# Performance work log

Measured on AMD Instinct MI355X. Metric: run time of the kernel, lower is better.

The kernel has to match this reference:

```python
import jax, jax.numpy as jnp
import numpy as np
import math

# ---- module hyperparameters (from init_kwargs) ----
N = 3            # polynomial points per segment
SEGMENTS = 512   # piecewise segments over [-1, 1] (length = 2.0)
ROTATIONS = 4    # -> 2*ROTATIONS stripe directions
WIDTH = 512
HEIGHT = 512
MAX_DIM = max(WIDTH, HEIGHT)
RATIO = MAX_DIM / (MAX_DIM + 1)
NUM_POS = 2 * ROTATIONS
NW = SEGMENTS * (N - 1) + 1  # continuous piecewise weights per channel

# Chebyshev-Lobatto interpolation points on [-1, 1]
CHEB = (-np.cos(np.pi * np.arange(N) / (N - 1))).astype(np.float32)


def make_positions():
    """Rotated stripe position maps, [2*ROTATIONS, WIDTH, HEIGHT], precomputed buffers."""
    xv, yv = np.meshgrid(np.arange(WIDTH), np.arange(HEIGHT), indexing='ij')
    xv = xv.astype(np.float32)
    yv = yv.astype(np.float32)
    pos = []
    for i in range(ROTATIONS):
        theta = math.pi / 2.0 * (i / ROTATIONS)
        cx, cy = math.cos(theta), math.sin(theta)
        for sgn in (1.0, -1.0):  # r1 = cx*x + cy*y, r2 = cx*x - cy*y
            r = cx * xv + sgn * cy * yv
            rmin, rmax = r.min(), r.max()
            dr = rmax - rmin
            r = ((r - rmin) * RATIO / dr - 0.5) * MAX_DIM
            pos.append(r)
    return np.stack(pos, 0).astype(np.float32)


POSITIONS = jnp.asarray(make_positions())  # [8, W, H] constant buffer


def lagrange_basis(t):
    """Lagrange basis at Chebyshev-Lobatto points; t [...], returns [..., N]."""
    bs = []
    for k in range(N):
        b = jnp.ones_like(t)
        for j in range(N):
            if j != k:
                b = b * (t - CHEB[j]) / (CHEB[k] - CHEB[j])
        bs.append(b)
    return jnp.stack(bs, axis=-1)


def piecewise_shared(xin, w):
    """Continuous piecewise Lagrange polynomial, weights shared across positions.
    xin: [B, C, L] in ~[-1, 1]; w: [C, NW]. Returns [B, C, L]."""
    xs = (xin + 1.0) * (0.5 * SEGMENTS)              # segment-space coordinate
    sid = jnp.clip(jnp.floor(xs), 0.0, SEGMENTS - 1)  # segment index (clamped)
    t = 2.0 * (xs - sid) - 1.0                        # local coord in [-1, 1]
    sid = sid.astype(jnp.int32)
    widx = sid[..., None] * (N - 1) + jnp.arange(N)   # [B, C, L, N] weight gather idx
    cidx = jnp.arange(w.shape[0])[None, :, None, None]
    wg = w[cidx, widx]                                # [B, C, L, N]
    return jnp.sum(lagrange_basis(t) * wg, axis=-1)


def setup_inputs() -> dict:
    key = jax.random.key(0)
    k1, k2 = jax.random.split(key)
    x = jax.random.normal(k1, (16, 3, WIDTH, HEIGHT), dtype=jnp.float32)
    weights = jax.random.normal(k2, (NUM_POS, 3, NW), dtype=jnp.float32)  # weight_magnitude=1
    return {"x": x, "weights": weights}


def reference(x, weights):
    B, C, W, H = x.shape
    accum = jnp.zeros((B, C, W * H), dtype=x.dtype)
    for i in range(NUM_POS):
        # position_encode: pixel value perturbs its stripe position, then rescale to [-1,1]
        dl = (0.5 * x + POSITIONS[i]) / (0.5 * MAX_DIM)  # [B, C, W, H]
        dl = dl.reshape(B, C, W * H)
        accum = accum + piecewise_shared(dl, weights[i])
    accum = accum / NUM_POS
    return accum.reshape(x.shape)
```

## Files before the change

kernel.cpp:

```cpp
#include <hip/hip_runtime.h>
#include <math.h>


#define WDIM 512
#define HDIM 512
#define SEGS 512
#define NPOS 8
#define NTAB 7
#define NW   1025
#define CCH  3

#define THREADS 512
#define TILE_X 128
#define TILE_Y 64
#define KITER  4
#define TILES_PER_SLICE ((WDIM / TILE_X) * (HDIM / TILE_Y))

struct Params {
    float ax[NPOS];
    float ay[NPOS];
    float c0[NPOS];
};

union HalfPack {
    unsigned int u;
    _Float16 h[2];
};

__global__ __launch_bounds__(THREADS, 6)
void stripe_poly_kernel(const float* __restrict__ x,
                        const float* __restrict__ w,
                        float* __restrict__ out,
                        Params P)
{
    __shared__ uint2 lut[NTAB][SEGS];

    const int slice = blockIdx.x / TILES_PER_SLICE;
    const int tile  = blockIdx.x % TILES_PER_SLICE;
    const int ch    = slice % CCH;
    const int bx    = (tile >> 3) * TILE_X;
    const int by    = (tile & 7) * TILE_Y;

    const int tid  = threadIdx.x;
    const int wv   = tid >> 6;
    const int lane = tid & 63;
    const int px0  = bx + (wv >> 2) * 16 + (lane >> 2);
    const int py   = by + (wv & 3) * 16 + (lane & 3) * 4;
    const float yf = (float)py;

    const size_t slice_off = (size_t)slice * (WDIM * HDIM);
    const size_t pbase = slice_off + (size_t)px0 * HDIM + py;

    const float4 xin0 = *(const float4*)(x + pbase);
    const float4 xin1 = *(const float4*)(x + pbase + (size_t)(1 * 32) * HDIM);
    const float4 xin2 = *(const float4*)(x + pbase + (size_t)(2 * 32) * HDIM);
    const float4 xin3 = *(const float4*)(x + pbase + (size_t)(3 * 32) * HDIM);

    for (int idx = threadIdx.x; idx < NTAB * SEGS; idx += THREADS) {
        const int m = idx >> 9;
        const int s = idx & (SEGS - 1);
        float w0, w1, w2;
        if (m == 0) {
            const float* wa = w + (size_t)(0 * CCH + ch) * NW + 2 * s;
            const float* wb = w + (size_t)(1 * CCH + ch) * NW + 2 * s;
            w0 = wa[0] + wb[0]; w1 = wa[1] + wb[1]; w2 = wa[2] + wb[2];
        } else {
            const float* wp = w + (size_t)((m + 1) * CCH + ch) * NW + 2 * s;
            w0 = wp[0]; w1 = wp[1]; w2 = wp[2];
        }
        const float a0 = 0.125f * w0;
        const float a1 = 0.125f * (fmaf(4.0f, w1, -w2) - 3.0f * w0);
        const float a2 = 0.25f  * (w0 - 2.0f * w1 + w2);
        HalfPack hp;
        hp.h[0] = (_Float16)a1;
        hp.h[1] = (_Float16)a2;
        lut[m][s] = make_uint2(__float_as_uint(a0), hp.u);
    }

    float gy[NTAB];
    #pragma unroll
    for (int i = 0; i < NTAB; ++i) {
        const int pi = (i == 0) ? 0 : (i + 1);
        gy[i] = fmaf(P.ay[pi], yf, P.c0[pi]);
    }

    __syncthreads();

    #pragma unroll
    for (int k = 0; k < KITER; ++k) {
        const size_t pk = pbase + (size_t)(k * 32) * HDIM;
        const float xf = (float)(px0 + k * 32);
        const float4 xk = (k == 0) ? xin0 : (k == 1) ? xin1 : (k == 2) ? xin2 : xin3;
        const float xv[4] = {xk.x, xk.y, xk.z, xk.w};
        float acc[4]  = {0.f, 0.f, 0.f, 0.f};
        float accC[4] = {0.f, 0.f, 0.f, 0.f};

        #pragma unroll
        for (int i = 0; i < NTAB; ++i) {
            const int pi = (i == 0) ? 0 : (i + 1);
            const float ay = P.ay[pi];
            const float g  = fmaf(P.ax[pi], xf, gy[i]);
            float gj[4];
            gj[0] = g;
            gj[1] = g + ay;
            gj[2] = gj[1] + ay;
            gj[3] = gj[2] + ay;
            #pragma unroll
            for (int j = 0; j < 4; ++j) {
                const float xs = fmaf(0.5f, xv[j], gj[j]);
                float sf = floorf(xs);
                sf = fminf(fmaxf(sf, 0.0f), (float)(SEGS - 1));
                const int s = (int)sf;
                const float d = xs - sf;
                const uint2 v = lut[i][s];
                HalfPack hp; hp.u = v.y;
                const float u = fmaf(d, (float)hp.h[1], (float)hp.h[0]);
                accC[j] += __uint_as_float(v.x);
                acc[j]   = fmaf(d, u, acc[j]);
            }
        }

        float4 o;
        o.x = acc[0] + accC[0];
        o.y = acc[1] + accC[1];
        o.z = acc[2] + accC[2];
        o.w = acc[3] + accC[3];
        *(float4*)(out + pk) = o;
    }
}

extern "C" void kernel_launch(void* const* d_in, const int* in_sizes, int n_in,
                              void* d_out, int out_size, void* d_ws, size_t ws_size,
                              hipStream_t stream)
{
    const float* x = (const float*)d_in[0];
    const float* w = (const float*)d_in[1];
    float* out = (float*)d_out;

    Params P;
    const double ratio_f = (double)(float)(512.0 / 513.0);
    for (int i = 0; i < 4; ++i) {
        const double theta = (M_PI * 0.5) * ((double)i / 4.0);
        const float a   = (float)cos(theta);
        const float cyf = (float)sin(theta);
        for (int sg = 0; sg < 2; ++sg) {
            const float b = (sg == 0) ? cyf : -cyf;
            const float ax511 = a * 511.0f;
            const float by511 = b * 511.0f;
            float rmin, rmax;
            if (sg == 0) { rmin = 0.0f;  rmax = ax511 + by511; }
            else         { rmin = by511; rmax = ax511; }
            const float dr = rmax - rmin;
            const double K = 512.0 * ratio_f / (double)dr;
            const int pi = 2 * i + sg;
            P.ax[pi] = (float)(K * (double)a);
            P.ay[pi] = (float)(K * (double)b);
            P.c0[pi] = (float)(-K * (double)rmin);
        }
    }

    const int slices = in_sizes[0] / (WDIM * HDIM);
    const int blocks = slices * TILES_PER_SLICE;
    stripe_poly_kernel<<<blocks, THREADS, 0, stream>>>(x, w, out, P);
}
```

Measured before the change: 119.6 us.

## Switch to fixed 1024-block grid that walks channel-grouped patches and restages LUT

Replaces the one-block-per-tile grid with a fixed grid of 1024 blocks. Each block processes 48 consecutive 16x16 patches ordered channel-major, so the coefficient LUT is built once per block and rebuilt only when the channel changes. Each iteration prefetches the next patch's input while computing the current one. The aim is to amortize the LUT staging from global weights over more pixels and to raise occupancy (launch bound 8). The trade-offs are that the patch count and channel layout are hardcoded for 16x3 slices, and the loop gains occasional extra barriers where a channel boundary falls inside a block.

```diff
diff --git a/kernel.cpp b/kernel.cpp
--- a/kernel.cpp
+++ b/kernel.cpp
@@ -11,10 +11,10 @@
 #define CCH  3
 
 #define THREADS 512
-#define TILE_X 128
-#define TILE_Y 64
-#define KITER  4
-#define TILES_PER_SLICE ((WDIM / TILE_X) * (HDIM / TILE_Y))
+#define BLOCKS  1024
+#define PER_BLK 48
+#define KITER   (PER_BLK / 8)
+#define PATCH_PER_CH 16384
 
 struct Params {
     float ax[NPOS];
@@ -27,7 +27,7 @@
     _Float16 h[2];
 };
 
-__global__ __launch_bounds__(THREADS, 6)
+__global__ __launch_bounds__(THREADS, 8)
 void stripe_poly_kernel(const float* __restrict__ x,
                         const float* __restrict__ w,
                         float* __restrict__ out,
@@ -35,63 +35,73 @@
 {
     __shared__ uint2 lut[NTAB][SEGS];
 
-    const int slice = blockIdx.x / TILES_PER_SLICE;
-    const int tile  = blockIdx.x % TILES_PER_SLICE;
-    const int ch    = slice % CCH;
-    const int bx    = (tile >> 3) * TILE_X;
-    const int by    = (tile & 7) * TILE_Y;
-
     const int tid  = threadIdx.x;
     const int wv   = tid >> 6;
     const int lane = tid & 63;
-    const int px0  = bx + (wv >> 2) * 16 + (lane >> 2);
-    const int py   = by + (wv & 3) * 16 + (lane & 3) * 4;
-    const float yf = (float)py;
+    const int plx  = lane >> 2;
+    const int ply  = (lane & 3) * 4;
 
-    const size_t slice_off = (size_t)slice * (WDIM * HDIM);
-    const size_t pbase = slice_off + (size_t)px0 * HDIM + py;
+    const int qbase = blockIdx.x * PER_BLK;
 
-    const float4 xin0 = *(const float4*)(x + pbase);
-    const float4 xin1 = *(const float4*)(x + pbase + (size_t)(1 * 32) * HDIM);
-    const float4 xin2 = *(const float4*)(x + pbase + (size_t)(2 * 32) * HDIM);
-    const float4 xin3 = *(const float4*)(x + pbase + (size_t)(3 * 32) * HDIM);
+    auto stage = [&](int ch) {
+        for (int idx = tid; idx < NTAB * SEGS; idx += THREADS) {
+            const int m = idx >> 9;
+            const int s = idx & (SEGS - 1);
+            float w0, w1, w2;
+            if (m == 0) {
+                const float* wa = w + (size_t)(0 * CCH + ch) * NW + 2 * s;
+                const float* wb = w + (size_t)(1 * CCH + ch) * NW + 2 * s;
+                w0 = wa[0] + wb[0]; w1 = wa[1] + wb[1]; w2 = wa[2] + wb[2];
+            } else {
+                const float* wp = w + (size_t)((m + 1) * CCH + ch) * NW + 2 * s;
+                w0 = wp[0]; w1 = wp[1]; w2 = wp[2];
+            }
+            const float a0 = 0.125f * w0;
+            const float a1 = 0.125f * (fmaf(4.0f, w1, -w2) - 3.0f * w0);
+            const float a2 = 0.25f  * (w0 - 2.0f * w1 + w2);
+            HalfPack hp;
+            hp.h[0] = (_Float16)a1;
+            hp.h[1] = (_Float16)a2;
+            lut[m][s] = make_uint2(__float_as_uint(a0), hp.u);
+        }
+    };
 
-    for (int idx = threadIdx.x; idx < NTAB * SEGS; idx += THREADS) {
-        const int m = idx >> 9;
-        const int s = idx & (SEGS - 1);
-        float w0, w1, w2;
-        if (m == 0) {
-            const float* wa = w + (size_t)(0 * CCH + ch) * NW + 2 * s;
-            const float* wb = w + (size_t)(1 * CCH + ch) * NW + 2 * s;
-            w0 = wa[0] + wb[0]; w1 = wa[1] + wb[1]; w2 = wa[2] + wb[2];
-        } else {
-            const float* wp = w + (size_t)((m + 1) * CCH + ch) * NW + 2 * s;
-            w0 = wp[0]; w1 = wp[1]; w2 = wp[2];
-        }
-        const float a0 = 0.125f * w0;
-        const float a1 = 0.125f * (fmaf(4.0f, w1, -w2) - 3.0f * w0);
-        const float a2 = 0.25f  * (w0 - 2.0f * w1 + w2);
-        HalfPack hp;
-        hp.h[0] = (_Float16)a1;
-        hp.h[1] = (_Float16)a2;
-        lut[m][s] = make_uint2(__float_as_uint(a0), hp.u);
-    }
+    auto coords = [&](int k, int& ch, float& xf, float& yf, size_t& off) {
+        const int q   = qbase + k * 8 + wv;
+        ch            = q >> 14;
+        const int r   = q & (PATCH_PER_CH - 1);
+        const int bsl = r >> 10;
+        const int pis = r & 1023;
+        const int px  = ((pis >> 5) << 4) + plx;
+        const int py  = ((pis & 31) << 4) + ply;
+        xf = (float)px; yf = (float)py;
+        off = ((size_t)(bsl * CCH + ch) << 18) + ((size_t)px << 9) + py;
+    };
 
-    float gy[NTAB];
-    #pragma unroll
-    for (int i = 0; i < NTAB; ++i) {
-        const int pi = (i == 0) ? 0 : (i + 1);
-        gy[i] = fmaf(P.ay[pi], yf, P.c0[pi]);
-    }
+    int c_cur = qbase >> 14;
+    stage(c_cur);
 
+    int ch0; float xf, yf; size_t off;
+    coords(0, ch0, xf, yf, off);
+    float4 xin = *(const float4*)(x + off);
     __syncthreads();
 
-    #pragma unroll
     for (int k = 0; k < KITER; ++k) {
-        const size_t pk = pbase + (size_t)(k * 32) * HDIM;
-        const float xf = (float)(px0 + k * 32);
-        const float4 xk = (k == 0) ? xin0 : (k == 1) ? xin1 : (k == 2) ? xin2 : xin3;
-        const float xv[4] = {xk.x, xk.y, xk.z, xk.w};
+        int chn; float xfn, yfn; size_t offn;
+        float4 xnext;
+        if (k + 1 < KITER) {
+            coords(k + 1, chn, xfn, yfn, offn);
+            xnext = *(const float4*)(x + offn);
+        }
+
+        if (ch0 != c_cur) {
+            __syncthreads();
+            stage(ch0);
+            c_cur = ch0;
+            __syncthreads();
+        }
+
+        const float xv[4] = {xin.x, xin.y, xin.z, xin.w};
         float acc[4]  = {0.f, 0.f, 0.f, 0.f};
         float accC[4] = {0.f, 0.f, 0.f, 0.f};
 
@@ -99,7 +109,7 @@
         for (int i = 0; i < NTAB; ++i) {
             const int pi = (i == 0) ? 0 : (i + 1);
             const float ay = P.ay[pi];
-            const float g  = fmaf(P.ax[pi], xf, gy[i]);
+            const float g  = fmaf(P.ax[pi], xf, fmaf(ay, yf, P.c0[pi]));
             float gj[4];
             gj[0] = g;
             gj[1] = g + ay;
@@ -125,7 +135,9 @@
         o.y = acc[1] + accC[1];
         o.z = acc[2] + accC[2];
         o.w = acc[3] + accC[3];
-        *(float4*)(out + pk) = o;
+        *(float4*)(out + off) = o;
+
+        xin = xnext; ch0 = chn; xf = xfn; yf = yfn; off = offn;
     }
 }
 
@@ -159,7 +171,5 @@
         }
     }
 
-    const int slices = in_sizes[0] / (WDIM * HDIM);
-    const int blocks = slices * TILES_PER_SLICE;
-    stripe_poly_kernel<<<blocks, THREADS, 0, stream>>>(x, w, out, P);
+    stripe_poly_kernel<<<BLOCKS, THREADS, 0, stream>>>(x, w, out, P);
 }
```

Measured after the change: 117.3 us. Within noise of the previous version (-1.9%).
